# Kernel tuning notes

Measured on AMD Instinct MI355X. Metric: run time of the kernel, lower is better.

The kernel has to match this reference:

```python
import jax, jax.numpy as jnp
import numpy as np

EPS = 1e-7


def setup_inputs() -> dict:
    key = jax.random.key(0)
    k1, k2, k3, k4 = jax.random.split(key, 4)
    S, N, R, CIN, COUT = 16, 1024, 4, 128, 128
    A = jax.random.uniform(k1, (S, N, N, R + 1), dtype=jnp.float32)
    x = jax.random.normal(k2, (S, N, CIN), dtype=jnp.float32)
    weight = jax.random.normal(k3, (CIN, COUT, R), dtype=jnp.float32) * 0.02
    theta_root = jax.random.normal(k4, (CIN, COUT), dtype=jnp.float32) * 0.02
    return {"A": A, "x": x, "weight": weight, "theta_root": theta_root}


def reference(A, x, weight, theta_root):
    # Drop the last relation channel ('no-edge' type in MolGAN)
    Ar = A[..., :-1]                                   # (s, N, N, R)
    # Per-destination, per-relation degree normalization
    norm = 1.0 / (jnp.sum(Ar, axis=2) + EPS)           # (s, N, R)
    # Fused contraction: avoid materializing Theta_ij (s,N,N,in,out).
    # x_new[s,i,b] = sum_{j,c,a} A[s,i,j,c] * norm[s,i,c] * x[s,j,a] * W[a,b,c]
    m = jnp.einsum('sijc,sja->sica', Ar, x)            # (s, N, R, in)
    m = m * norm[..., None]                            # apply norm over (s,i,c)
    agg = jnp.einsum('sica,abc->sib', m, weight)       # (s, N, out)
    x_new = agg + x @ theta_root                       # root/self term
    return jnp.tanh(x_new)
```

## Files before the change

kernel.cpp:

```cpp
#include <hip/hip_runtime.h>
#include <hip/hip_bf16.h>
#include <math.h>

#define SS    16
#define NN    1024
#define RR    4
#define CINC  128
#define COUTC 128
#define RP1   5
#define EPSF  1e-7f

typedef __bf16 bf16x8 __attribute__((ext_vector_type(8)));
typedef __bf16 bf16x4 __attribute__((ext_vector_type(4)));
typedef float  f32x4  __attribute__((ext_vector_type(4)));

#define YT_BYTES ((size_t)SS * RR * COUTC * NN * 2)
#define Z_BYTES  ((size_t)SS * NN * COUTC * 4)
#define XB_BYTES ((size_t)SS * NN * CINC * 2)

__global__ __launch_bounds__(256) void convert_kernel(
    const float* __restrict__ x, const float* __restrict__ weight,
    const float* __restrict__ theta, __bf16* __restrict__ xb,
    __bf16* __restrict__ wT)
{
    const int bx = blockIdx.x, t = threadIdx.x;
    if (bx < 1024) {
        const size_t e0 = ((size_t)bx * 256 + t) * 8;
        f32x4 v0 = *(const f32x4*)(x + e0);
        f32x4 v1 = *(const f32x4*)(x + e0 + 4);
        bf16x8 o;
        o[0] = (__bf16)v0.x; o[1] = (__bf16)v0.y; o[2] = (__bf16)v0.z; o[3] = (__bf16)v0.w;
        o[4] = (__bf16)v1.x; o[5] = (__bf16)v1.y; o[6] = (__bf16)v1.z; o[7] = (__bf16)v1.w;
        *(bf16x8*)(xb + e0) = o;
    } else if (t < 128) {
        const int a = bx - 1024;
        f32x4 wv = *(const f32x4*)(weight + ((size_t)a * COUTC + t) * RR);
        wT[(0 * COUTC + t) * CINC + a] = (__bf16)wv.x;
        wT[(1 * COUTC + t) * CINC + a] = (__bf16)wv.y;
        wT[(2 * COUTC + t) * CINC + a] = (__bf16)wv.z;
        wT[(3 * COUTC + t) * CINC + a] = (__bf16)wv.w;
        wT[(4 * COUTC + t) * CINC + a] = (__bf16)theta[(size_t)a * COUTC + t];
    }
}

__global__ __launch_bounds__(256) void prep_kernel(
    const __bf16* __restrict__ xb, const __bf16* __restrict__ wT,
    __bf16* __restrict__ Yt, float* __restrict__ Z)
{
    const int bx = blockIdx.x;
    const int s  = bx & 15;
    const int r  = bx >> 4;
    const int ch = r % 5;
    const int jt = r / 5;

    const int t = threadIdx.x, lane = t & 63, w = t >> 6;
    const int m16 = lane & 15, quad = lane >> 4;

    const __bf16* xrow = xb + ((size_t)(s * NN) + jt * 64 + w * 16 + m16) * CINC;
    const __bf16* wch  = wT + (size_t)ch * COUTC * CINC;

    f32x4 acc[8];
#pragma unroll
    for (int i = 0; i < 8; ++i) acc[i] = (f32x4){0.f, 0.f, 0.f, 0.f};

#pragma unroll
    for (int k0 = 0; k0 < CINC; k0 += 32) {
        const bf16x8 af = *(const bf16x8*)(xrow + k0 + quad * 8);
#pragma unroll
        for (int bs = 0; bs < 8; ++bs) {
            const bf16x8 bf = *(const bf16x8*)(wch + (size_t)(bs * 16 + m16) * CINC + k0 + quad * 8);
            acc[bs] = __builtin_amdgcn_mfma_f32_16x16x32_bf16(af, bf, acc[bs], 0, 0, 0);
        }
    }

    const int j0 = jt * 64 + w * 16 + quad * 4;
    if (ch < 4) {
#pragma unroll
        for (int bs = 0; bs < 8; ++bs) {
            const int b = bs * 16 + m16;
            bf16x4 v; v[0] = (__bf16)acc[bs][0]; v[1] = (__bf16)acc[bs][1];
                      v[2] = (__bf16)acc[bs][2]; v[3] = (__bf16)acc[bs][3];
            *(bf16x4*)(Yt + ((size_t)((s * 4 + ch) * COUTC + b)) * NN + j0) = v;
        }
    } else {
#pragma unroll
        for (int bs = 0; bs < 8; ++bs) {
            const int b = bs * 16 + m16;
#pragma unroll
            for (int r4 = 0; r4 < 4; ++r4)
                Z[((size_t)s * NN + j0 + r4) * COUTC + b] = acc[bs][r4];
        }
    }
}

__global__ __launch_bounds__(256, 2) void main_kernel(
    const float* __restrict__ A, const __bf16* __restrict__ Yt,
    const float* __restrict__ Z, float* __restrict__ out)
{
    const int bx = blockIdx.x;
    const int s  = bx & 15;
    const int i0 = (bx >> 4) * 32;

    __shared__ __bf16 lA[2][4][32][40];
    __shared__ float  lnorm[4][32];

    const int t = threadIdx.x;
    const int lane = t & 63, w = t >> 6;
    const int m16 = lane & 15, quad = lane >> 4;

    const int irow = t >> 3;
    const int q    = t & 7;

    const float* Ap = A + ((size_t)(s * NN + i0 + irow) * NN) * RP1 + q * 20;

    float rs[4] = {0.f, 0.f, 0.f, 0.f};
    f32x4 acc[4][2][2];
#pragma unroll
    for (int c = 0; c < 4; ++c)
#pragma unroll
        for (int is = 0; is < 2; ++is)
#pragma unroll
            for (int bs = 0; bs < 2; ++bs) acc[c][is][bs] = (f32x4){0.f, 0.f, 0.f, 0.f};

    const __bf16* Ys = Yt + (size_t)s * 4 * COUTC * NN;

    f32x4 ld[5];
#pragma unroll
    for (int u = 0; u < 5; ++u) ld[u] = __builtin_nontemporal_load((const f32x4*)Ap + u);

    for (int kk = 0; kk < 32; ++kk) {
        const int p = kk & 1;

        {
            const float v0[4] = {ld[0].x, ld[1].y, ld[2].z, ld[3].w};
            const float v1[4] = {ld[0].y, ld[1].z, ld[2].w, ld[4].x};
            const float v2[4] = {ld[0].z, ld[1].w, ld[3].x, ld[4].y};
            const float v3[4] = {ld[0].w, ld[2].x, ld[3].y, ld[4].z};
            const float* vv[4] = {v0, v1, v2, v3};
#pragma unroll
            for (int c = 0; c < 4; ++c) {
                const float* v = vv[c];
                rs[c] += v[0] + v[1] + v[2] + v[3];
                bf16x4 pk; pk[0] = (__bf16)v[0]; pk[1] = (__bf16)v[1];
                           pk[2] = (__bf16)v[2]; pk[3] = (__bf16)v[3];
                *(bf16x4*)&lA[p][c][irow][q * 4] = pk;
            }
        }
        __syncthreads();

        if (kk < 31) {
            Ap += 160;
#pragma unroll
            for (int u = 0; u < 5; ++u) ld[u] = __builtin_nontemporal_load((const f32x4*)Ap + u);
        }

        bf16x8 bf[4][2];
        const __bf16* yp = Ys + kk * 32 + quad * 8;
#pragma unroll
        for (int c = 0; c < 4; ++c)
#pragma unroll
            for (int bs = 0; bs < 2; ++bs)
                bf[c][bs] = *(const bf16x8*)(yp + (size_t)(c * COUTC + w * 32 + bs * 16 + m16) * NN);

#pragma unroll
        for (int c = 0; c < 4; ++c) {
            const bf16x8 af0 = *(const bf16x8*)&lA[p][c][m16][quad * 8];
            const bf16x8 af1 = *(const bf16x8*)&lA[p][c][16 + m16][quad * 8];
            acc[c][0][0] = __builtin_amdgcn_mfma_f32_16x16x32_bf16(af0, bf[c][0], acc[c][0][0], 0, 0, 0);
            acc[c][0][1] = __builtin_amdgcn_mfma_f32_16x16x32_bf16(af0, bf[c][1], acc[c][0][1], 0, 0, 0);
            acc[c][1][0] = __builtin_amdgcn_mfma_f32_16x16x32_bf16(af1, bf[c][0], acc[c][1][0], 0, 0, 0);
            acc[c][1][1] = __builtin_amdgcn_mfma_f32_16x16x32_bf16(af1, bf[c][1], acc[c][1][1], 0, 0, 0);
        }
    }

#pragma unroll
    for (int c = 0; c < 4; ++c) {
        float v = rs[c];
        v += __shfl_xor(v, 1);
        v += __shfl_xor(v, 2);
        v += __shfl_xor(v, 4);
        if (q == 0) lnorm[c][irow] = 1.0f / (v + EPSF);
    }
    __syncthreads();

#pragma unroll
    for (int is = 0; is < 2; ++is) {
        f32x4 nv[4];
#pragma unroll
        for (int c = 0; c < 4; ++c) nv[c] = *(const f32x4*)&lnorm[c][is * 16 + quad * 4];
        const int row0 = i0 + is * 16 + quad * 4;
#pragma unroll
        for (int bs = 0; bs < 2; ++bs) {
            const int b = w * 32 + bs * 16 + m16;
#pragma unroll
            for (int r = 0; r < 4; ++r) {
                float v = acc[0][is][bs][r] * nv[0][r]
                        + acc[1][is][bs][r] * nv[1][r]
                        + acc[2][is][bs][r] * nv[2][r]
                        + acc[3][is][bs][r] * nv[3][r];
                const size_t idx = ((size_t)s * NN + row0 + r) * COUTC + b;
                out[idx] = tanhf(v + Z[idx]);
            }
        }
    }
}

extern "C" void kernel_launch(void* const* d_in, const int* in_sizes, int n_in,
                              void* d_out, int out_size, void* d_ws, size_t ws_size,
                              hipStream_t stream)
{
    const float* A      = (const float*)d_in[0];
    const float* x      = (const float*)d_in[1];
    const float* weight = (const float*)d_in[2];
    const float* theta  = (const float*)d_in[3];
    float* out = (float*)d_out;

    __bf16* Yt = (__bf16*)d_ws;
    float*  Z  = (float*)((char*)d_ws + YT_BYTES);
    __bf16* xb = (__bf16*)((char*)d_ws + YT_BYTES + Z_BYTES);
    __bf16* wT = (__bf16*)((char*)d_ws + YT_BYTES + Z_BYTES + XB_BYTES);

    convert_kernel<<<dim3(1024 + 128), dim3(256), 0, stream>>>(x, weight, theta, xb, wT);
    prep_kernel<<<dim3(SS * 5 * 16), dim3(256), 0, stream>>>(xb, wT, Yt, Z);
    main_kernel<<<dim3(SS * 32), dim3(256), 0, stream>>>(A, Yt, Z, out);
}
```

Measured before the change: 585.9 us.

## Fuse root term into main kernel, drop x bf16 copy, halve row tile

Removes the separate bf16 conversion of x and the fp32 Z buffer: prep now converts x on the fly, and the main kernel computes the x@theta_root term itself with MFMA before the A loop. The main kernel tile drops from 32 to 16 destination rows, giving 1024 blocks with occupancy hint 4 and a 64-wide k step per iteration. This cuts workspace traffic and launch work, and improves parallelism over CUs for the memory-bound A stream. In exchange, Yt is reread by twice as many blocks and per-block work per A byte changes.

Result: slower. 608.1 us (+3.8%).

```diff
diff --git a/kernel.cpp b/kernel.cpp
--- a/kernel.cpp
+++ b/kernel.cpp
@@ -15,48 +15,35 @@
 typedef float  f32x4  __attribute__((ext_vector_type(4)));
 
 #define YT_BYTES ((size_t)SS * RR * COUTC * NN * 2)
-#define Z_BYTES  ((size_t)SS * NN * COUTC * 4)
-#define XB_BYTES ((size_t)SS * NN * CINC * 2)
 
 __global__ __launch_bounds__(256) void convert_kernel(
-    const float* __restrict__ x, const float* __restrict__ weight,
-    const float* __restrict__ theta, __bf16* __restrict__ xb,
+    const float* __restrict__ weight, const float* __restrict__ theta,
     __bf16* __restrict__ wT)
 {
-    const int bx = blockIdx.x, t = threadIdx.x;
-    if (bx < 1024) {
-        const size_t e0 = ((size_t)bx * 256 + t) * 8;
-        f32x4 v0 = *(const f32x4*)(x + e0);
-        f32x4 v1 = *(const f32x4*)(x + e0 + 4);
-        bf16x8 o;
-        o[0] = (__bf16)v0.x; o[1] = (__bf16)v0.y; o[2] = (__bf16)v0.z; o[3] = (__bf16)v0.w;
-        o[4] = (__bf16)v1.x; o[5] = (__bf16)v1.y; o[6] = (__bf16)v1.z; o[7] = (__bf16)v1.w;
-        *(bf16x8*)(xb + e0) = o;
-    } else if (t < 128) {
-        const int a = bx - 1024;
-        f32x4 wv = *(const f32x4*)(weight + ((size_t)a * COUTC + t) * RR);
-        wT[(0 * COUTC + t) * CINC + a] = (__bf16)wv.x;
-        wT[(1 * COUTC + t) * CINC + a] = (__bf16)wv.y;
-        wT[(2 * COUTC + t) * CINC + a] = (__bf16)wv.z;
-        wT[(3 * COUTC + t) * CINC + a] = (__bf16)wv.w;
-        wT[(4 * COUTC + t) * CINC + a] = (__bf16)theta[(size_t)a * COUTC + t];
-    }
+    const int idx = blockIdx.x * 256 + threadIdx.x;
+    const int a = idx >> 7, b = idx & 127;
+    f32x4 wv = *(const f32x4*)(weight + ((size_t)a * COUTC + b) * RR);
+    wT[(0 * COUTC + b) * CINC + a] = (__bf16)wv.x;
+    wT[(1 * COUTC + b) * CINC + a] = (__bf16)wv.y;
+    wT[(2 * COUTC + b) * CINC + a] = (__bf16)wv.z;
+    wT[(3 * COUTC + b) * CINC + a] = (__bf16)wv.w;
+    wT[(4 * COUTC + b) * CINC + a] = (__bf16)theta[(size_t)a * COUTC + b];
 }
 
 __global__ __launch_bounds__(256) void prep_kernel(
-    const __bf16* __restrict__ xb, const __bf16* __restrict__ wT,
-    __bf16* __restrict__ Yt, float* __restrict__ Z)
+    const float* __restrict__ x, const __bf16* __restrict__ wT,
+    __bf16* __restrict__ Yt)
 {
     const int bx = blockIdx.x;
     const int s  = bx & 15;
     const int r  = bx >> 4;
-    const int ch = r % 5;
-    const int jt = r / 5;
+    const int ch = r & 3;
+    const int jt = r >> 2;
 
     const int t = threadIdx.x, lane = t & 63, w = t >> 6;
     const int m16 = lane & 15, quad = lane >> 4;
 
-    const __bf16* xrow = xb + ((size_t)(s * NN) + jt * 64 + w * 16 + m16) * CINC;
+    const float*  xrow = x  + ((size_t)(s * NN) + jt * 64 + w * 16 + m16) * CINC;
     const __bf16* wch  = wT + (size_t)ch * COUTC * CINC;
 
     f32x4 acc[8];
@@ -65,7 +52,11 @@
 
 #pragma unroll
     for (int k0 = 0; k0 < CINC; k0 += 32) {
-        const bf16x8 af = *(const bf16x8*)(xrow + k0 + quad * 8);
+        f32x4 xa = *(const f32x4*)(xrow + k0 + quad * 8);
+        f32x4 xc = *(const f32x4*)(xrow + k0 + quad * 8 + 4);
+        bf16x8 af;
+        af[0] = (__bf16)xa.x; af[1] = (__bf16)xa.y; af[2] = (__bf16)xa.z; af[3] = (__bf16)xa.w;
+        af[4] = (__bf16)xc.x; af[5] = (__bf16)xc.y; af[6] = (__bf16)xc.z; af[7] = (__bf16)xc.w;
 #pragma unroll
         for (int bs = 0; bs < 8; ++bs) {
             const bf16x8 bf = *(const bf16x8*)(wch + (size_t)(bs * 16 + m16) * CINC + k0 + quad * 8);
@@ -74,53 +65,63 @@
     }
 
     const int j0 = jt * 64 + w * 16 + quad * 4;
-    if (ch < 4) {
-#pragma unroll
-        for (int bs = 0; bs < 8; ++bs) {
-            const int b = bs * 16 + m16;
-            bf16x4 v; v[0] = (__bf16)acc[bs][0]; v[1] = (__bf16)acc[bs][1];
-                      v[2] = (__bf16)acc[bs][2]; v[3] = (__bf16)acc[bs][3];
-            *(bf16x4*)(Yt + ((size_t)((s * 4 + ch) * COUTC + b)) * NN + j0) = v;
-        }
-    } else {
-#pragma unroll
-        for (int bs = 0; bs < 8; ++bs) {
-            const int b = bs * 16 + m16;
-#pragma unroll
-            for (int r4 = 0; r4 < 4; ++r4)
-                Z[((size_t)s * NN + j0 + r4) * COUTC + b] = acc[bs][r4];
-        }
-    }
-}
-
-__global__ __launch_bounds__(256, 2) void main_kernel(
-    const float* __restrict__ A, const __bf16* __restrict__ Yt,
-    const float* __restrict__ Z, float* __restrict__ out)
+#pragma unroll
+    for (int bs = 0; bs < 8; ++bs) {
+        const int b = bs * 16 + m16;
+        bf16x4 v; v[0] = (__bf16)acc[bs][0]; v[1] = (__bf16)acc[bs][1];
+                  v[2] = (__bf16)acc[bs][2]; v[3] = (__bf16)acc[bs][3];
+        *(bf16x4*)(Yt + ((size_t)((s * 4 + ch) * COUTC + b)) * NN + j0) = v;
+    }
+}
+
+__global__ __launch_bounds__(256, 4) void main_kernel(
+    const float* __restrict__ A, const float* __restrict__ x,
+    const __bf16* __restrict__ Yt, const __bf16* __restrict__ wT,
+    float* __restrict__ out)
 {
     const int bx = blockIdx.x;
     const int s  = bx & 15;
-    const int i0 = (bx >> 4) * 32;
-
-    __shared__ __bf16 lA[2][4][32][40];
-    __shared__ float  lnorm[4][32];
+    const int i0 = (bx >> 4) * 16;
+
+    __shared__ __bf16 lA[2][4][16][72];
+    __shared__ float  lnorm[4][16];
 
     const int t = threadIdx.x;
     const int lane = t & 63, w = t >> 6;
     const int m16 = lane & 15, quad = lane >> 4;
 
-    const int irow = t >> 3;
-    const int q    = t & 7;
+    const int irow = t >> 4;
+    const int q    = t & 15;
 
     const float* Ap = A + ((size_t)(s * NN + i0 + irow) * NN) * RP1 + q * 20;
 
+    f32x4 accz[2];
+    accz[0] = (f32x4){0.f, 0.f, 0.f, 0.f};
+    accz[1] = (f32x4){0.f, 0.f, 0.f, 0.f};
+    {
+        const float*  xrow = x  + ((size_t)(s * NN) + i0 + m16) * CINC;
+        const __bf16* wth  = wT + (size_t)4 * COUTC * CINC;
+#pragma unroll
+        for (int k0 = 0; k0 < CINC; k0 += 32) {
+            f32x4 xa = *(const f32x4*)(xrow + k0 + quad * 8);
+            f32x4 xc = *(const f32x4*)(xrow + k0 + quad * 8 + 4);
+            bf16x8 af;
+            af[0] = (__bf16)xa.x; af[1] = (__bf16)xa.y; af[2] = (__bf16)xa.z; af[3] = (__bf16)xa.w;
+            af[4] = (__bf16)xc.x; af[5] = (__bf16)xc.y; af[6] = (__bf16)xc.z; af[7] = (__bf16)xc.w;
+#pragma unroll
+            for (int bs = 0; bs < 2; ++bs) {
+                const bf16x8 bf = *(const bf16x8*)(wth + (size_t)(w * 32 + bs * 16 + m16) * CINC + k0 + quad * 8);
+                accz[bs] = __builtin_amdgcn_mfma_f32_16x16x32_bf16(af, bf, accz[bs], 0, 0, 0);
+            }
+        }
+    }
+
     float rs[4] = {0.f, 0.f, 0.f, 0.f};
-    f32x4 acc[4][2][2];
+    f32x4 acc[4][2];
 #pragma unroll
     for (int c = 0; c < 4; ++c)
 #pragma unroll
-        for (int is = 0; is < 2; ++is)
-#pragma unroll
-            for (int bs = 0; bs < 2; ++bs) acc[c][is][bs] = (f32x4){0.f, 0.f, 0.f, 0.f};
+        for (int bs = 0; bs < 2; ++bs) acc[c][bs] = (f32x4){0.f, 0.f, 0.f, 0.f};
 
     const __bf16* Ys = Yt + (size_t)s * 4 * COUTC * NN;
 
@@ -128,7 +129,7 @@
 #pragma unroll
     for (int u = 0; u < 5; ++u) ld[u] = __builtin_nontemporal_load((const f32x4*)Ap + u);
 
-    for (int kk = 0; kk < 32; ++kk) {
+    for (int kk = 0; kk < 16; ++kk) {
         const int p = kk & 1;
 
         {
@@ -148,28 +149,23 @@
         }
         __syncthreads();
 
-        if (kk < 31) {
-            Ap += 160;
+        if (kk < 15) {
+            Ap += 320;
 #pragma unroll
             for (int u = 0; u < 5; ++u) ld[u] = __builtin_nontemporal_load((const f32x4*)Ap + u);
         }
 
-        bf16x8 bf[4][2];
-        const __bf16* yp = Ys + kk * 32 + quad * 8;
-#pragma unroll
-        for (int c = 0; c < 4; ++c)
-#pragma unroll
-            for (int bs = 0; bs < 2; ++bs)
-                bf[c][bs] = *(const bf16x8*)(yp + (size_t)(c * COUTC + w * 32 + bs * 16 + m16) * NN);
-
 #pragma unroll
         for (int c = 0; c < 4; ++c) {
-            const bf16x8 af0 = *(const bf16x8*)&lA[p][c][m16][quad * 8];
-            const bf16x8 af1 = *(const bf16x8*)&lA[p][c][16 + m16][quad * 8];
-            acc[c][0][0] = __builtin_amdgcn_mfma_f32_16x16x32_bf16(af0, bf[c][0], acc[c][0][0], 0, 0, 0);
-            acc[c][0][1] = __builtin_amdgcn_mfma_f32_16x16x32_bf16(af0, bf[c][1], acc[c][0][1], 0, 0, 0);
-            acc[c][1][0] = __builtin_amdgcn_mfma_f32_16x16x32_bf16(af1, bf[c][0], acc[c][1][0], 0, 0, 0);
-            acc[c][1][1] = __builtin_amdgcn_mfma_f32_16x16x32_bf16(af1, bf[c][1], acc[c][1][1], 0, 0, 0);
+            const __bf16* yp = Ys + (size_t)(c * COUTC + w * 32 + m16) * NN + kk * 64 + quad * 8;
+#pragma unroll
+            for (int ks = 0; ks < 2; ++ks) {
+                const bf16x8 af = *(const bf16x8*)&lA[p][c][m16][ks * 32 + quad * 8];
+                const bf16x8 b0 = *(const bf16x8*)(yp + ks * 32);
+                const bf16x8 b1 = *(const bf16x8*)(yp + (size_t)16 * NN + ks * 32);
+                acc[c][0] = __builtin_amdgcn_mfma_f32_16x16x32_bf16(af, b0, acc[c][0], 0, 0, 0);
+                acc[c][1] = __builtin_amdgcn_mfma_f32_16x16x32_bf16(af, b1, acc[c][1], 0, 0, 0);
+            }
         }
     }
 
@@ -179,27 +175,27 @@
         v += __shfl_xor(v, 1);
         v += __shfl_xor(v, 2);
         v += __shfl_xor(v, 4);
+        v += __shfl_xor(v, 8);
         if (q == 0) lnorm[c][irow] = 1.0f / (v + EPSF);
     }
     __syncthreads();
 
-#pragma unroll
-    for (int is = 0; is < 2; ++is) {
+    {
         f32x4 nv[4];
 #pragma unroll
-        for (int c = 0; c < 4; ++c) nv[c] = *(const f32x4*)&lnorm[c][is * 16 + quad * 4];
-        const int row0 = i0 + is * 16 + quad * 4;
+        for (int c = 0; c < 4; ++c) nv[c] = *(const f32x4*)&lnorm[c][quad * 4];
+        const int row0 = i0 + quad * 4;
 #pragma unroll
         for (int bs = 0; bs < 2; ++bs) {
             const int b = w * 32 + bs * 16 + m16;
 #pragma unroll
             for (int r = 0; r < 4; ++r) {
-                float v = acc[0][is][bs][r] * nv[0][r]
-                        + acc[1][is][bs][r] * nv[1][r]
-                        + acc[2][is][bs][r] * nv[2][r]
-                        + acc[3][is][bs][r] * nv[3][r];
-                const size_t idx = ((size_t)s * NN + row0 + r) * COUTC + b;
-                out[idx] = tanhf(v + Z[idx]);
+                float v = acc[0][bs][r] * nv[0][r]
+                        + acc[1][bs][r] * nv[1][r]
+                        + acc[2][bs][r] * nv[2][r]
+                        + acc[3][bs][r] * nv[3][r]
+                        + accz[bs][r];
+                out[((size_t)s * NN + row0 + r) * COUTC + b] = tanhf(v);
             }
         }
     }
@@ -216,11 +212,9 @@
     float* out = (float*)d_out;
 
     __bf16* Yt = (__bf16*)d_ws;
-    float*  Z  = (float*)((char*)d_ws + YT_BYTES);
-    __bf16* xb = (__bf16*)((char*)d_ws + YT_BYTES + Z_BYTES);
-    __bf16* wT = (__bf16*)((char*)d_ws + YT_BYTES + Z_BYTES + XB_BYTES);
-
-    convert_kernel<<<dim3(1024 + 128), dim3(256), 0, stream>>>(x, weight, theta, xb, wT);
-    prep_kernel<<<dim3(SS * 5 * 16), dim3(256), 0, stream>>>(xb, wT, Yt, Z);
-    main_kernel<<<dim3(SS * 32), dim3(256), 0, stream>>>(A, Yt, Z, out);
-}
+    __bf16* wT = (__bf16*)((char*)d_ws + YT_BYTES);
+
+    convert_kernel<<<dim3(64), dim3(256), 0, stream>>>(weight, theta, wT);
+    prep_kernel<<<dim3(SS * RR * 16), dim3(256), 0, stream>>>(x, wT, Yt);
+    main_kernel<<<dim3(SS * 64), dim3(256), 0, stream>>>(A, x, Yt, wT, out);
+}
```
